# Kernel optimization log

Measured on AMD Instinct MI355X. Metric: run time of the kernel, lower is better.

Reference implementation:

```python
import jax, jax.numpy as jnp
import numpy as np

BN, SN = 16, 64
C, T, FY, FX = 480, 8, 28, 28
OS = 8            # roialign output_size
NDF = 256
K = 64            # n_clusters
ALPHA = 1.0
IMG_W, IMG_H = 1920.0, 1080.0
SPATIAL_SCALE = 1.0


def _roi_align(feat, boxes):
    """torchvision RoIAlign with sampling_ratio=1, aligned=True.
    feat: [bn, C, H, W]; boxes: [bn, sn, 4] (x1,y1,x2,y2) in feature coords.
    Returns [bn, sn, C, OS, OS]."""
    bn, c, H, W = feat.shape
    xy1 = boxes[..., 0:2] * SPATIAL_SCALE - 0.5   # aligned=True offset
    xy2 = boxes[..., 2:4] * SPATIAL_SCALE - 0.5
    bin_wh = (xy2 - xy1) / OS                     # [bn,sn,2]
    ctr = jnp.arange(OS, dtype=feat.dtype) + 0.5  # one sample per bin (ratio=1)
    xs = xy1[..., 0:1] + ctr * bin_wh[..., 0:1]   # [bn,sn,OS]
    ys = xy1[..., 1:2] + ctr * bin_wh[..., 1:2]
    X = xs[:, :, None, :]                         # [bn,sn,1,OS]
    Y = ys[:, :, :, None]                         # [bn,sn,OS,1]
    valid = (Y > -1.0) & (Y < H) & (X > -1.0) & (X < W)
    x = jnp.clip(X, 0.0, W - 1.0)
    y = jnp.clip(Y, 0.0, H - 1.0)
    x0 = jnp.floor(x).astype(jnp.int32)
    y0 = jnp.floor(y).astype(jnp.int32)
    x1 = jnp.minimum(x0 + 1, W - 1)
    y1 = jnp.minimum(y0 + 1, H - 1)
    lx = x - x0
    ly = y - y0
    fhw = jnp.transpose(feat, (0, 2, 3, 1))       # [bn,H,W,C]
    g = jax.vmap(lambda f, yy, xx: f[yy, xx])     # broadcasting gather -> [bn,sn,OS,OS,C]
    v00 = g(fhw, y0, x0); v01 = g(fhw, y0, x1)
    v10 = g(fhw, y1, x0); v11 = g(fhw, y1, x1)
    wy0, wy1 = (1.0 - ly)[..., None], ly[..., None]
    wx0, wx1 = (1.0 - lx)[..., None], lx[..., None]
    out = v00 * wy0 * wx0 + v01 * wy0 * wx1 + v10 * wy1 * wx0 + v11 * wy1 * wx1
    out = jnp.where(valid[..., None], out, 0.0)
    return jnp.transpose(out, (0, 1, 4, 2, 3))    # [bn,sn,C,OS,OS] (torch layout)


def setup_inputs() -> dict:
    key = jax.random.key(0)
    ks = jax.random.split(key, 6)
    z_vis = jax.random.normal(ks[0], (BN, C, T, FY, FX), jnp.float32)
    # valid boxes (x1<x2, y1<y2), fully inside the image -> no NaN padding rows
    tl = jax.random.uniform(ks[1], (BN, SN, 2)) * jnp.array([IMG_W * 0.5, IMG_H * 0.5])
    wh = jax.random.uniform(ks[2], (BN, SN, 2)) * jnp.array([IMG_W * 0.4, IMG_H * 0.4]) + 16.0
    bboxs = jnp.concatenate([tl, tl + wh], axis=-1).astype(jnp.float32)
    W_vis = jax.random.normal(ks[3], (C * OS * OS, NDF), jnp.float32) / np.sqrt(C * OS * OS)
    b_vis = jnp.zeros((NDF,), jnp.float32)
    W_spc = jax.random.normal(ks[4], (1, NDF), jnp.float32)
    b_spc = jnp.zeros((NDF,), jnp.float32)
    centroids = jax.random.normal(ks[5], (K, NDF), jnp.float32) * 0.1
    return {"z_vis": z_vis, "bboxs": bboxs, "W_vis": W_vis, "b_vis": b_vis,
            "W_spc": W_spc, "b_spc": b_spc, "centroids": centroids}


def reference(z_vis, bboxs, W_vis, b_vis, W_spc, b_spc, centroids):
    bn, sn = bboxs.shape[:2]
    # scale image-coord boxes to feature-map coords
    scale = jnp.array([FX / IMG_W, FY / IMG_H], dtype=z_vis.dtype)
    boxes_f = (bboxs.reshape(bn, sn, 2, 2) * scale).reshape(bn, sn, 4)
    feat = z_vis[:, :, -1]                                   # last temporal frame [bn,C,fy,fx]
    roi = _roi_align(feat, boxes_f).reshape(bn, sn, -1)      # [bn,sn,C*OS*OS]
    z_v = roi @ W_vis + b_vis                                # visual embedding [bn,sn,NDF]
    # spatial embedding: normalized distance of bbox center to image center (detached)
    b2 = bboxs.reshape(bn, sn, 2, 2)
    ctr = b2[:, :, 0] + (b2[:, :, 1] - b2[:, :, 0]) * 0.5    # [bn,sn,2]
    img_c = jnp.array([IMG_W / 2.0, IMG_H / 2.0], dtype=z_vis.dtype)
    norms = jnp.linalg.norm(ctr - img_c, axis=-1, keepdims=True) / jnp.linalg.norm(img_c)
    norms = jax.lax.stop_gradient(norms)                     # .detach() in original
    z_s = norms @ W_spc + b_spc                              # [bn,sn,NDF]
    z = z_v + z_s
    # Student-t soft assignment on L2 distance (NOT squared, as in the source)
    d = jnp.linalg.norm(z[:, :, None, :] - centroids, axis=-1)   # [bn,sn,K]
    s_un = (1.0 + d / ALPHA) ** (-(ALPHA + 1.0) / 2.0)
    s = s_un / jnp.sum(s_un, axis=-1, keepdims=True)
    c = jnp.argmax(s, axis=-1)
    return z, s, c
```

## Files before the change

### kernel.cpp

```cpp
#include <hip/hip_runtime.h>
#include <cstdint>
#include <cstddef>

#define BN_   16
#define C_    480
#define T_    8
#define FY_   28
#define FX_   28
#define NDF_  256
#define KC_   64
#define M_    1024
#define KD_   30720
#define PLANE_ 784
#define CHSTRIDE_ (T_*PLANE_)
#define CT_   (C_*CHSTRIDE_)
#define KS_   32
#define KCH_  960
#define NCH_  15
#define NSTEP_ 30
#define MT_   64
#define AOS_  520
#define BTILE_ 16384

typedef __attribute__((ext_vector_type(8))) short bf16x8;
typedef __attribute__((ext_vector_type(4))) float f32x4;

__device__ __forceinline__ unsigned rne_bf16(float f) {
    union { float f; unsigned u; } v; v.f = f;
    return v.u + 0x7FFFu + ((v.u >> 16) & 1u);
}
__device__ __forceinline__ float bfbits_to_f(unsigned r) {
    union { unsigned u; float f; } v; v.u = r & 0xFFFF0000u;
    return v.f;
}
__device__ __forceinline__ void lds_dma16(const void* g, void* l) {
    __builtin_amdgcn_global_load_lds((const __attribute__((address_space(1))) void*)g,
                                     (__attribute__((address_space(3))) void*)l, 16, 0, 0);
}

__global__ __launch_bounds__(256)
void convert_pack(const float* __restrict__ W, unsigned short* __restrict__ Bpack) {
    const int blk = blockIdx.x;
    const int kb = blk * 32;
    const int n = threadIdx.x;
    unsigned hw[16], lw[16];
    #pragma unroll
    for (int p = 0; p < 16; ++p) {
        const float v0 = W[(size_t)(kb + 2 * p) * NDF_ + n];
        const float v1 = W[(size_t)(kb + 2 * p + 1) * NDF_ + n];
        const unsigned h0 = rne_bf16(v0), h1 = rne_bf16(v1);
        const unsigned l0 = rne_bf16(v0 - bfbits_to_f(h0));
        const unsigned l1 = rne_bf16(v1 - bfbits_to_f(h1));
        hw[p] = __builtin_amdgcn_perm(h1, h0, 0x07060302u);
        lw[p] = __builtin_amdgcn_perm(l1, l0, 0x07060302u);
    }
    uint4* hb4 = (uint4*)(Bpack + (size_t)blk * BTILE_);
    uint4* lb4 = hb4 + 1024;
    #pragma unroll
    for (int o = 0; o < 4; ++o) {
        hb4[o * 256 + n] = make_uint4(hw[o * 4 + 0], hw[o * 4 + 1], hw[o * 4 + 2], hw[o * 4 + 3]);
        lb4[o * 256 + n] = make_uint4(lw[o * 4 + 0], lw[o * 4 + 1], lw[o * 4 + 2], lw[o * 4 + 3]);
    }
}

__global__ void convert_cent(const float* __restrict__ cent, float* __restrict__ centT) {
    const int k = blockIdx.x;
    const int j = threadIdx.x;
    centT[(size_t)j * KC_ + k] = cent[(size_t)k * NDF_ + j];
}

__global__ __launch_bounds__(256, 2)
void gemm_fused(const float* __restrict__ z_vis, const unsigned short* __restrict__ Bpack,
                const float* __restrict__ bboxs, float* __restrict__ z_part) {
    __shared__ short Ah[8 * AOS_];
    __shared__ short Al[8 * AOS_];
    __shared__ unsigned short Bh[8192];
    __shared__ unsigned short Bl[8192];
    __shared__ float Pl[PLANE_];

    const int t = threadIdx.x;
    const int ks = blockIdx.x, mi = blockIdx.y;
    const int lane = t & 63, wid = t >> 6;

    const int m = t >> 2, byl = t & 3;
    const int roi = mi * MT_ + m;

    int xi0[8], xi1[8];
    float xw0[8], xw1[8];
    int yr0[2], yr1[2];
    float wy0[2], wy1[2];
    {
        const float bx1 = bboxs[roi * 4 + 0], by1 = bboxs[roi * 4 + 1];
        const float bx2 = bboxs[roi * 4 + 2], by2 = bboxs[roi * 4 + 3];
        const float sx = 28.0f / 1920.0f, sy = 28.0f / 1080.0f;
        const float lo_x = bx1 * sx - 0.5f;
        const float binw_x = (bx2 * sx - 0.5f - lo_x) * 0.125f;
        const float lo_y = by1 * sy - 0.5f;
        const float binw_y = (by2 * sy - 0.5f - lo_y) * 0.125f;
        #pragma unroll
        for (int b = 0; b < 8; ++b) {
            const float pos = lo_x + ((float)b + 0.5f) * binw_x;
            const float vx = (pos > -1.0f && pos < 28.0f) ? 1.0f : 0.0f;
            const float pc = fminf(fmaxf(pos, 0.0f), 27.0f);
            const float p0 = floorf(pc);
            const float lx = pc - p0;
            xi0[b] = (int)p0;
            xi1[b] = min(xi0[b] + 1, 27);
            xw0[b] = vx * (1.0f - lx);
            xw1[b] = vx * lx;
        }
        #pragma unroll
        for (int h = 0; h < 2; ++h) {
            const int by = byl + h * 4;
            const float pos = lo_y + ((float)by + 0.5f) * binw_y;
            const float vy = (pos > -1.0f && pos < 28.0f) ? 1.0f : 0.0f;
            const float pc = fminf(fmaxf(pos, 0.0f), 27.0f);
            const float p0 = floorf(pc);
            const float ly = pc - p0;
            const int y0 = (int)p0, y1 = min(y0 + 1, 27);
            yr0[h] = y0 * FX_; yr1[h] = y1 * FX_;
            wy0[h] = vy * (1.0f - ly); wy1[h] = vy * ly;
        }
    }
    const float* plane = z_vis + (size_t)mi * CT_ + (size_t)(T_ - 1) * PLANE_;

    auto plane_load = [&](int cc) {
        const char* gb = (const char*)(plane + (size_t)(ks * NCH_ + cc) * CHSTRIDE_);
        if (wid < 3) {
            lds_dma16(gb + (wid * 64 + lane) * 16, (char*)Pl + wid * 1024);
        } else if (lane < 4) {
            lds_dma16(gb + (192 + lane) * 16, (char*)Pl + 3072);
        }
    };

    auto stage_B = [&](int s) {
        const char* hb = (const char*)(Bpack + (size_t)(ks * NSTEP_ + s) * BTILE_);
        #pragma unroll
        for (int qq = 0; qq < 4; ++qq) {
            const int chunk = (qq * 4 + wid) * 1024;
            lds_dma16(hb + chunk + lane * 16, (char*)Bh + chunk);
            lds_dma16(hb + 16384 + chunk + lane * 16, (char*)Bl + chunk);
        }
    };

    auto stage_A = [&]() {
        #pragma unroll
        for (int h = 0; h < 2; ++h) {
            const int by = byl + h * 4;
            const int r0 = yr0[h], r1 = yr1[h];
            const float w0 = wy0[h], w1 = wy1[h];
            unsigned rh[8], rl[8];
            #pragma unroll
            for (int b = 0; b < 8; ++b) {
                const float v00 = Pl[r0 + xi0[b]], v01 = Pl[r0 + xi1[b]];
                const float v10 = Pl[r1 + xi0[b]], v11 = Pl[r1 + xi1[b]];
                const float val = w0 * (xw0[b] * v00 + xw1[b] * v01)
                                + w1 * (xw0[b] * v10 + xw1[b] * v11);
                rh[b] = rne_bf16(val);
                rl[b] = rne_bf16(val - bfbits_to_f(rh[b]));
            }
            const uint4 hh = make_uint4(__builtin_amdgcn_perm(rh[1], rh[0], 0x07060302u),
                                        __builtin_amdgcn_perm(rh[3], rh[2], 0x07060302u),
                                        __builtin_amdgcn_perm(rh[5], rh[4], 0x07060302u),
                                        __builtin_amdgcn_perm(rh[7], rh[6], 0x07060302u));
            const uint4 ll = make_uint4(__builtin_amdgcn_perm(rl[1], rl[0], 0x07060302u),
                                        __builtin_amdgcn_perm(rl[3], rl[2], 0x07060302u),
                                        __builtin_amdgcn_perm(rl[5], rl[4], 0x07060302u),
                                        __builtin_amdgcn_perm(rl[7], rl[6], 0x07060302u));
            *(uint4*)&Ah[by * AOS_ + m * 8] = hh;
            *(uint4*)&Al[by * AOS_ + m * 8] = ll;
        }
    };

    const int fr = lane & 15, fq = lane >> 4;
    f32x4 acc[4][4] = {};

    plane_load(0);
    stage_B(0);
    __syncthreads();
    stage_A();

    for (int cc = 0; cc < NCH_; ++cc) {
        #pragma unroll
        for (int half = 0; half < 2; ++half) {
            const int s = 2 * cc + half;
            __syncthreads();

            bf16x8 afh[4], afl[4], bh[4], bl[4];
            #pragma unroll
            for (int i = 0; i < 4; ++i) {
                const int ao = (half * 4 + fq) * AOS_ + (i * 16 + fr) * 8;
                afh[i] = *(const bf16x8*)&Ah[ao];
                afl[i] = *(const bf16x8*)&Al[ao];
            }
            #pragma unroll
            for (int j = 0; j < 4; ++j) {
                const int bo = fq * 2048 + (wid * 64 + j * 16 + fr) * 8;
                bh[j] = *(const bf16x8*)&Bh[bo];
                bl[j] = *(const bf16x8*)&Bl[bo];
            }
            __syncthreads();

            if (half == 0) {
                stage_B(s + 1);
                if (cc + 1 < NCH_) plane_load(cc + 1);
            } else if (cc + 1 < NCH_) {
                stage_B(s + 1);
                stage_A();
            }

            #pragma unroll
            for (int j = 0; j < 4; ++j)
                #pragma unroll
                for (int i = 0; i < 4; ++i) {
                    acc[i][j] = __builtin_amdgcn_mfma_f32_16x16x32_bf16(afh[i], bh[j], acc[i][j], 0, 0, 0);
                    acc[i][j] = __builtin_amdgcn_mfma_f32_16x16x32_bf16(afl[i], bh[j], acc[i][j], 0, 0, 0);
                    acc[i][j] = __builtin_amdgcn_mfma_f32_16x16x32_bf16(afh[i], bl[j], acc[i][j], 0, 0, 0);
                }
        }
    }

    float* zp = z_part + (size_t)ks * (M_ * NDF_);
    #pragma unroll
    for (int i = 0; i < 4; ++i) {
        const int row = mi * MT_ + i * 16 + fq * 4;
        #pragma unroll
        for (int j = 0; j < 4; ++j) {
            const int col = wid * 64 + j * 16 + fr;
            #pragma unroll
            for (int r = 0; r < 4; ++r)
                zp[(size_t)(row + r) * NDF_ + col] = acc[i][j][r];
        }
    }
}

__global__ __launch_bounds__(256)
void cluster_kernel(const float* __restrict__ z_part, const float* __restrict__ bboxs,
                    const float* __restrict__ b_vis, const float* __restrict__ W_spc,
                    const float* __restrict__ b_spc, const float* __restrict__ centT,
                    float* __restrict__ out) {
    const int row = blockIdx.x, t = threadIdx.x;
    __shared__ float zs[NDF_];
    __shared__ float dp[4][KC_];

    float a = 0.0f;
    const float* zp = z_part + (size_t)row * NDF_ + t;
    #pragma unroll
    for (int s = 0; s < KS_; ++s)
        a += zp[(size_t)s * (M_ * NDF_)];

    const float x1 = bboxs[row * 4 + 0], y1 = bboxs[row * 4 + 1];
    const float x2 = bboxs[row * 4 + 2], y2 = bboxs[row * 4 + 3];
    const float cx = x1 + (x2 - x1) * 0.5f - 960.0f;
    const float cy = y1 + (y2 - y1) * 0.5f - 540.0f;
    const float nrm = sqrtf(cx * cx + cy * cy) / sqrtf(960.0f * 960.0f + 540.0f * 540.0f);

    const float zj = a + b_vis[t] + nrm * W_spc[t] + b_spc[t];
    zs[t] = zj;
    out[(size_t)row * NDF_ + t] = zj;
    __syncthreads();

    const int k = t & 63, qq = t >> 6;
    {
        float d2 = 0.0f;
        const float* ct = centT + (size_t)qq * 64 * KC_;
        #pragma unroll 8
        for (int j = 0; j < 64; ++j) {
            const float df = zs[qq * 64 + j] - ct[(size_t)j * KC_ + k];
            d2 += df * df;
        }
        dp[qq][k] = d2;
    }
    __syncthreads();

    if (t < 64) {
        const float d = sqrtf(dp[0][t] + dp[1][t] + dp[2][t] + dp[3][t]);
        const float su = 1.0f / (1.0f + d);
        float sum = su;
        #pragma unroll
        for (int mk = 1; mk < 64; mk <<= 1) sum += __shfl_xor(sum, mk, 64);
        out[(size_t)M_ * NDF_ + (size_t)row * KC_ + t] = su / sum;
        float v = d; int idx = t;
        #pragma unroll
        for (int mk = 1; mk < 64; mk <<= 1) {
            const float ov = __shfl_xor(v, mk, 64);
            const int oi = __shfl_xor(idx, mk, 64);
            if (ov < v || (ov == v && oi < idx)) { v = ov; idx = oi; }
        }
        if (t == 0)
            out[(size_t)M_ * NDF_ + (size_t)M_ * KC_ + row] = (float)idx;
    }
}

extern "C" void kernel_launch(void* const* d_in, const int* in_sizes, int n_in,
                              void* d_out, int out_size, void* d_ws, size_t ws_size,
                              hipStream_t stream) {
    const float* z_vis = (const float*)d_in[0];
    const float* bboxs = (const float*)d_in[1];
    const float* W_vis = (const float*)d_in[2];
    const float* b_vis = (const float*)d_in[3];
    const float* W_spc = (const float*)d_in[4];
    const float* b_spc = (const float*)d_in[5];
    const float* cent  = (const float*)d_in[6];
    float* out = (float*)d_out;

    char* ws = (char*)d_ws;
    unsigned short* Bpack = (unsigned short*)ws;
    float*          centT = (float*)(ws + 31457280);
    float*          z_part = (float*)(ws + 31457280 + 65536);

    convert_pack<<<KS_ * NSTEP_, 256, 0, stream>>>(W_vis, Bpack);
    convert_cent<<<KC_, 256, 0, stream>>>(cent, centT);
    gemm_fused<<<dim3(KS_, M_ / MT_), 256, 0, stream>>>(z_vis, Bpack, bboxs, z_part);
    cluster_kernel<<<M_, 256, 0, stream>>>(z_part, bboxs, b_vis, W_spc, b_spc, centT, out);
}
```

Before: 331.2 us.

## Split GEMM block into 8 waves and reorder split-K partial layout

The fused RoIAlign+GEMM kernel now runs 512 threads per block, with waves arranged 2x4 over the M and N tile, so each wave holds half as many accumulators. The A-staging work per thread and the B-staging loop are split across the larger thread count. The z_part partial buffer is relaid out as row-major [row][ks][col], so the cluster kernel's split-K reduction reads contiguous memory instead of striding across whole planes. This aims at better latency hiding and lower register pressure, but each wave now reloads the B fragments, and the launch bound of 4 blocks of 512 threads may not fit given the LDS use.

```diff
diff --git a/kernel.cpp b/kernel.cpp
--- a/kernel.cpp
+++ b/kernel.cpp
@@ -69,7 +69,7 @@
     centT[(size_t)j * KC_ + k] = cent[(size_t)k * NDF_ + j];
 }
 
-__global__ __launch_bounds__(256, 2)
+__global__ __launch_bounds__(512, 4)
 void gemm_fused(const float* __restrict__ z_vis, const unsigned short* __restrict__ Bpack,
                 const float* __restrict__ bboxs, float* __restrict__ z_part) {
     __shared__ short Ah[8 * AOS_];
@@ -81,14 +81,15 @@
     const int t = threadIdx.x;
     const int ks = blockIdx.x, mi = blockIdx.y;
     const int lane = t & 63, wid = t >> 6;
-
-    const int m = t >> 2, byl = t & 3;
+    const int wm = wid >> 2, wn = wid & 3;
+
+    const int m = t >> 3, by = t & 7;
     const int roi = mi * MT_ + m;
 
     int xi0[8], xi1[8];
     float xw0[8], xw1[8];
-    int yr0[2], yr1[2];
-    float wy0[2], wy1[2];
+    int yr0, yr1;
+    float wy0, wy1;
     {
         const float bx1 = bboxs[roi * 4 + 0], by1 = bboxs[roi * 4 + 1];
         const float bx2 = bboxs[roi * 4 + 2], by2 = bboxs[roi * 4 + 3];
@@ -109,17 +110,15 @@
             xw0[b] = vx * (1.0f - lx);
             xw1[b] = vx * lx;
         }
-        #pragma unroll
-        for (int h = 0; h < 2; ++h) {
-            const int by = byl + h * 4;
+        {
             const float pos = lo_y + ((float)by + 0.5f) * binw_y;
             const float vy = (pos > -1.0f && pos < 28.0f) ? 1.0f : 0.0f;
             const float pc = fminf(fmaxf(pos, 0.0f), 27.0f);
             const float p0 = floorf(pc);
             const float ly = pc - p0;
             const int y0 = (int)p0, y1 = min(y0 + 1, 27);
-            yr0[h] = y0 * FX_; yr1[h] = y1 * FX_;
-            wy0[h] = vy * (1.0f - ly); wy1[h] = vy * ly;
+            yr0 = y0 * FX_; yr1 = y1 * FX_;
+            wy0 = vy * (1.0f - ly); wy1 = vy * ly;
         }
     }
     const float* plane = z_vis + (size_t)mi * CT_ + (size_t)(T_ - 1) * PLANE_;
@@ -128,7 +127,7 @@
         const char* gb = (const char*)(plane + (size_t)(ks * NCH_ + cc) * CHSTRIDE_);
         if (wid < 3) {
             lds_dma16(gb + (wid * 64 + lane) * 16, (char*)Pl + wid * 1024);
-        } else if (lane < 4) {
+        } else if (wid == 3 && lane < 4) {
             lds_dma16(gb + (192 + lane) * 16, (char*)Pl + 3072);
         }
     };
@@ -136,44 +135,40 @@
     auto stage_B = [&](int s) {
         const char* hb = (const char*)(Bpack + (size_t)(ks * NSTEP_ + s) * BTILE_);
         #pragma unroll
-        for (int qq = 0; qq < 4; ++qq) {
-            const int chunk = (qq * 4 + wid) * 1024;
+        for (int qq = 0; qq < 2; ++qq) {
+            const int chunk = (qq * 8 + wid) * 1024;
             lds_dma16(hb + chunk + lane * 16, (char*)Bh + chunk);
             lds_dma16(hb + 16384 + chunk + lane * 16, (char*)Bl + chunk);
         }
     };
 
     auto stage_A = [&]() {
-        #pragma unroll
-        for (int h = 0; h < 2; ++h) {
-            const int by = byl + h * 4;
-            const int r0 = yr0[h], r1 = yr1[h];
-            const float w0 = wy0[h], w1 = wy1[h];
-            unsigned rh[8], rl[8];
-            #pragma unroll
-            for (int b = 0; b < 8; ++b) {
-                const float v00 = Pl[r0 + xi0[b]], v01 = Pl[r0 + xi1[b]];
-                const float v10 = Pl[r1 + xi0[b]], v11 = Pl[r1 + xi1[b]];
-                const float val = w0 * (xw0[b] * v00 + xw1[b] * v01)
-                                + w1 * (xw0[b] * v10 + xw1[b] * v11);
-                rh[b] = rne_bf16(val);
-                rl[b] = rne_bf16(val - bfbits_to_f(rh[b]));
-            }
-            const uint4 hh = make_uint4(__builtin_amdgcn_perm(rh[1], rh[0], 0x07060302u),
-                                        __builtin_amdgcn_perm(rh[3], rh[2], 0x07060302u),
-                                        __builtin_amdgcn_perm(rh[5], rh[4], 0x07060302u),
-                                        __builtin_amdgcn_perm(rh[7], rh[6], 0x07060302u));
-            const uint4 ll = make_uint4(__builtin_amdgcn_perm(rl[1], rl[0], 0x07060302u),
-                                        __builtin_amdgcn_perm(rl[3], rl[2], 0x07060302u),
-                                        __builtin_amdgcn_perm(rl[5], rl[4], 0x07060302u),
-                                        __builtin_amdgcn_perm(rl[7], rl[6], 0x07060302u));
-            *(uint4*)&Ah[by * AOS_ + m * 8] = hh;
-            *(uint4*)&Al[by * AOS_ + m * 8] = ll;
-        }
+        const int r0 = yr0, r1 = yr1;
+        const float w0 = wy0, w1 = wy1;
+        unsigned rh[8], rl[8];
+        #pragma unroll
+        for (int b = 0; b < 8; ++b) {
+            const float v00 = Pl[r0 + xi0[b]], v01 = Pl[r0 + xi1[b]];
+            const float v10 = Pl[r1 + xi0[b]], v11 = Pl[r1 + xi1[b]];
+            const float val = w0 * (xw0[b] * v00 + xw1[b] * v01)
+                            + w1 * (xw0[b] * v10 + xw1[b] * v11);
+            rh[b] = rne_bf16(val);
+            rl[b] = rne_bf16(val - bfbits_to_f(rh[b]));
+        }
+        const uint4 hh = make_uint4(__builtin_amdgcn_perm(rh[1], rh[0], 0x07060302u),
+                                    __builtin_amdgcn_perm(rh[3], rh[2], 0x07060302u),
+                                    __builtin_amdgcn_perm(rh[5], rh[4], 0x07060302u),
+                                    __builtin_amdgcn_perm(rh[7], rh[6], 0x07060302u));
+        const uint4 ll = make_uint4(__builtin_amdgcn_perm(rl[1], rl[0], 0x07060302u),
+                                    __builtin_amdgcn_perm(rl[3], rl[2], 0x07060302u),
+                                    __builtin_amdgcn_perm(rl[5], rl[4], 0x07060302u),
+                                    __builtin_amdgcn_perm(rl[7], rl[6], 0x07060302u));
+        *(uint4*)&Ah[by * AOS_ + m * 8] = hh;
+        *(uint4*)&Al[by * AOS_ + m * 8] = ll;
     };
 
     const int fr = lane & 15, fq = lane >> 4;
-    f32x4 acc[4][4] = {};
+    f32x4 acc[2][4] = {};
 
     plane_load(0);
     stage_B(0);
@@ -186,16 +181,16 @@
             const int s = 2 * cc + half;
             __syncthreads();
 
-            bf16x8 afh[4], afl[4], bh[4], bl[4];
+            bf16x8 afh[2], afl[2], bh[4], bl[4];
             #pragma unroll
-            for (int i = 0; i < 4; ++i) {
-                const int ao = (half * 4 + fq) * AOS_ + (i * 16 + fr) * 8;
+            for (int i = 0; i < 2; ++i) {
+                const int ao = (half * 4 + fq) * AOS_ + (wm * 32 + i * 16 + fr) * 8;
                 afh[i] = *(const bf16x8*)&Ah[ao];
                 afl[i] = *(const bf16x8*)&Al[ao];
             }
             #pragma unroll
             for (int j = 0; j < 4; ++j) {
-                const int bo = fq * 2048 + (wid * 64 + j * 16 + fr) * 8;
+                const int bo = fq * 2048 + (wn * 64 + j * 16 + fr) * 8;
                 bh[j] = *(const bf16x8*)&Bh[bo];
                 bl[j] = *(const bf16x8*)&Bl[bo];
             }
@@ -212,7 +207,7 @@
             #pragma unroll
             for (int j = 0; j < 4; ++j)
                 #pragma unroll
-                for (int i = 0; i < 4; ++i) {
+                for (int i = 0; i < 2; ++i) {
                     acc[i][j] = __builtin_amdgcn_mfma_f32_16x16x32_bf16(afh[i], bh[j], acc[i][j], 0, 0, 0);
                     acc[i][j] = __builtin_amdgcn_mfma_f32_16x16x32_bf16(afl[i], bh[j], acc[i][j], 0, 0, 0);
                     acc[i][j] = __builtin_amdgcn_mfma_f32_16x16x32_bf16(afh[i], bl[j], acc[i][j], 0, 0, 0);
@@ -220,16 +215,15 @@
         }
     }
 
-    float* zp = z_part + (size_t)ks * (M_ * NDF_);
     #pragma unroll
-    for (int i = 0; i < 4; ++i) {
-        const int row = mi * MT_ + i * 16 + fq * 4;
+    for (int i = 0; i < 2; ++i) {
+        const int row = mi * MT_ + wm * 32 + i * 16 + fq * 4;
         #pragma unroll
         for (int j = 0; j < 4; ++j) {
-            const int col = wid * 64 + j * 16 + fr;
+            const int col = wn * 64 + j * 16 + fr;
             #pragma unroll
             for (int r = 0; r < 4; ++r)
-                zp[(size_t)(row + r) * NDF_ + col] = acc[i][j][r];
+                z_part[((size_t)(row + r) * KS_ + ks) * NDF_ + col] = acc[i][j][r];
         }
     }
 }
@@ -244,10 +238,10 @@
     __shared__ float dp[4][KC_];
 
     float a = 0.0f;
-    const float* zp = z_part + (size_t)row * NDF_ + t;
+    const float* zp = z_part + (size_t)row * (KS_ * NDF_) + t;
     #pragma unroll
     for (int s = 0; s < KS_; ++s)
-        a += zp[(size_t)s * (M_ * NDF_)];
+        a += zp[(size_t)s * NDF_];
 
     const float x1 = bboxs[row * 4 + 0], y1 = bboxs[row * 4 + 1];
     const float x2 = bboxs[row * 4 + 2], y2 = bboxs[row * 4 + 3];
@@ -311,6 +305,6 @@
 
     convert_pack<<<KS_ * NSTEP_, 256, 0, stream>>>(W_vis, Bpack);
     convert_cent<<<KC_, 256, 0, stream>>>(cent, centT);
-    gemm_fused<<<dim3(KS_, M_ / MT_), 256, 0, stream>>>(z_vis, Bpack, bboxs, z_part);
+    gemm_fused<<<dim3(KS_, M_ / MT_), 512, 0, stream>>>(z_vis, Bpack, bboxs, z_part);
     cluster_kernel<<<M_, 256, 0, stream>>>(z_part, bboxs, b_vis, W_spc, b_spc, centT, out);
 }
```

Measured after the change: 348.3 us. 5.2% more time.

## Fuse weight bf16 split-packing into GEMM B staging and drop centroid transpose

Applied to the files above, without the earlier changes.

Removes the separate convert_pack and convert_cent kernels. The GEMM now reads fp32 W_vis directly in stage_B and does the hi/lo bf16 split inside the block before writing to LDS, instead of DMA-ing a prepacked buffer. The cluster kernel reads centroids in their original layout, with per-thread contiguous rows. This saves two launches and a full write-then-read pass over the packed weights. The cost is that each of the 16 M-tile blocks redoes the conversion, reads twice the bytes of W through the cache, and uses synchronous loads instead of async LDS DMA, which may break load/compute overlap.

```diff
diff --git a/kernel.cpp b/kernel.cpp
--- a/kernel.cpp
+++ b/kernel.cpp
@@ -20,7 +20,6 @@
 #define NSTEP_ 30
 #define MT_   64
 #define AOS_  520
-#define BTILE_ 16384
 
 typedef __attribute__((ext_vector_type(8))) short bf16x8;
 typedef __attribute__((ext_vector_type(4))) float f32x4;
@@ -38,39 +37,8 @@
                                      (__attribute__((address_space(3))) void*)l, 16, 0, 0);
 }
 
-__global__ __launch_bounds__(256)
-void convert_pack(const float* __restrict__ W, unsigned short* __restrict__ Bpack) {
-    const int blk = blockIdx.x;
-    const int kb = blk * 32;
-    const int n = threadIdx.x;
-    unsigned hw[16], lw[16];
-    #pragma unroll
-    for (int p = 0; p < 16; ++p) {
-        const float v0 = W[(size_t)(kb + 2 * p) * NDF_ + n];
-        const float v1 = W[(size_t)(kb + 2 * p + 1) * NDF_ + n];
-        const unsigned h0 = rne_bf16(v0), h1 = rne_bf16(v1);
-        const unsigned l0 = rne_bf16(v0 - bfbits_to_f(h0));
-        const unsigned l1 = rne_bf16(v1 - bfbits_to_f(h1));
-        hw[p] = __builtin_amdgcn_perm(h1, h0, 0x07060302u);
-        lw[p] = __builtin_amdgcn_perm(l1, l0, 0x07060302u);
-    }
-    uint4* hb4 = (uint4*)(Bpack + (size_t)blk * BTILE_);
-    uint4* lb4 = hb4 + 1024;
-    #pragma unroll
-    for (int o = 0; o < 4; ++o) {
-        hb4[o * 256 + n] = make_uint4(hw[o * 4 + 0], hw[o * 4 + 1], hw[o * 4 + 2], hw[o * 4 + 3]);
-        lb4[o * 256 + n] = make_uint4(lw[o * 4 + 0], lw[o * 4 + 1], lw[o * 4 + 2], lw[o * 4 + 3]);
-    }
-}
-
-__global__ void convert_cent(const float* __restrict__ cent, float* __restrict__ centT) {
-    const int k = blockIdx.x;
-    const int j = threadIdx.x;
-    centT[(size_t)j * KC_ + k] = cent[(size_t)k * NDF_ + j];
-}
-
 __global__ __launch_bounds__(256, 2)
-void gemm_fused(const float* __restrict__ z_vis, const unsigned short* __restrict__ Bpack,
+void gemm_fused(const float* __restrict__ z_vis, const float* __restrict__ W,
                 const float* __restrict__ bboxs, float* __restrict__ z_part) {
     __shared__ short Ah[8 * AOS_];
     __shared__ short Al[8 * AOS_];
@@ -134,12 +102,22 @@
     };
 
     auto stage_B = [&](int s) {
-        const char* hb = (const char*)(Bpack + (size_t)(ks * NSTEP_ + s) * BTILE_);
-        #pragma unroll
-        for (int qq = 0; qq < 4; ++qq) {
-            const int chunk = (qq * 4 + wid) * 1024;
-            lds_dma16(hb + chunk + lane * 16, (char*)Bh + chunk);
-            lds_dma16(hb + 16384 + chunk + lane * 16, (char*)Bl + chunk);
+        const float* wsrc = W + (size_t)(ks * NSTEP_ + s) * 32 * NDF_ + t;
+        #pragma unroll
+        for (int o = 0; o < 4; ++o) {
+            unsigned hw[4], lw[4];
+            #pragma unroll
+            for (int p = 0; p < 4; ++p) {
+                const float v0 = wsrc[(size_t)(o * 8 + 2 * p) * NDF_];
+                const float v1 = wsrc[(size_t)(o * 8 + 2 * p + 1) * NDF_];
+                const unsigned h0 = rne_bf16(v0), h1 = rne_bf16(v1);
+                const unsigned l0 = rne_bf16(v0 - bfbits_to_f(h0));
+                const unsigned l1 = rne_bf16(v1 - bfbits_to_f(h1));
+                hw[p] = __builtin_amdgcn_perm(h1, h0, 0x07060302u);
+                lw[p] = __builtin_amdgcn_perm(l1, l0, 0x07060302u);
+            }
+            *(uint4*)&Bh[o * 2048 + t * 8] = make_uint4(hw[0], hw[1], hw[2], hw[3]);
+            *(uint4*)&Bl[o * 2048 + t * 8] = make_uint4(lw[0], lw[1], lw[2], lw[3]);
         }
     };
 
@@ -237,7 +215,7 @@
 __global__ __launch_bounds__(256)
 void cluster_kernel(const float* __restrict__ z_part, const float* __restrict__ bboxs,
                     const float* __restrict__ b_vis, const float* __restrict__ W_spc,
-                    const float* __restrict__ b_spc, const float* __restrict__ centT,
+                    const float* __restrict__ b_spc, const float* __restrict__ cent,
                     float* __restrict__ out) {
     const int row = blockIdx.x, t = threadIdx.x;
     __shared__ float zs[NDF_];
@@ -263,10 +241,10 @@
     const int k = t & 63, qq = t >> 6;
     {
         float d2 = 0.0f;
-        const float* ct = centT + (size_t)qq * 64 * KC_;
+        const float* ct = cent + (size_t)k * NDF_ + qq * 64;
         #pragma unroll 8
         for (int j = 0; j < 64; ++j) {
-            const float df = zs[qq * 64 + j] - ct[(size_t)j * KC_ + k];
+            const float df = zs[qq * 64 + j] - ct[j];
             d2 += df * df;
         }
         dp[qq][k] = d2;
@@ -305,12 +283,8 @@
     float* out = (float*)d_out;
 
     char* ws = (char*)d_ws;
-    unsigned short* Bpack = (unsigned short*)ws;
-    float*          centT = (float*)(ws + 31457280);
-    float*          z_part = (float*)(ws + 31457280 + 65536);
-
-    convert_pack<<<KS_ * NSTEP_, 256, 0, stream>>>(W_vis, Bpack);
-    convert_cent<<<KC_, 256, 0, stream>>>(cent, centT);
-    gemm_fused<<<dim3(KS_, M_ / MT_), 256, 0, stream>>>(z_vis, Bpack, bboxs, z_part);
-    cluster_kernel<<<M_, 256, 0, stream>>>(z_part, bboxs, b_vis, W_spc, b_spc, centT, out);
-}
+    float* z_part = (float*)ws;
+
+    gemm_fused<<<dim3(KS_, M_ / MT_), 256, 0, stream>>>(z_vis, W_vis, bboxs, z_part);
+    cluster_kernel<<<M_, 256, 0, stream>>>(z_part, bboxs, b_vis, W_spc, b_spc, cent, out);
+}
```

Result: slower. 493.5 us (+49.0%).
